# Optimization experiments

Hardware: AMD Instinct MI355X
Metric: run time of the kernel (lower is better)

## Reference

```python
import jax, jax.numpy as jnp
import numpy as np

B, C, H, W = 64, 3, 224, 224
DEPTH = 2
NUM_OPS = 14

def _lin(m, lo, hi):
    return lo + m * (hi - lo)

def _clip255(x):
    return jnp.clip(x, 0.0, 255.0)

def _affine_sample(img, a, b, c, d, e, f):
    # img: [C,H,W]; inverse map (x_out,y_out)->(a*x+b*y+c, d*x+e*y+f); bilinear, zero fill.
    ch, h, w = img.shape
    ys, xs = jnp.meshgrid(jnp.arange(h, dtype=img.dtype), jnp.arange(w, dtype=img.dtype), indexing='ij')
    sx = a * xs + b * ys + c
    sy = d * xs + e * ys + f
    x0 = jnp.floor(sx); y0 = jnp.floor(sy)
    wx = sx - x0; wy = sy - y0
    def gather(yi, xi):
        valid = (xi >= 0) & (xi <= w - 1) & (yi >= 0) & (yi <= h - 1)
        v = img[:, jnp.clip(yi, 0, h - 1).astype(jnp.int32), jnp.clip(xi, 0, w - 1).astype(jnp.int32)]
        return jnp.where(valid[None], v, 0.0)
    v00 = gather(y0, x0); v01 = gather(y0, x0 + 1)
    v10 = gather(y0 + 1, x0); v11 = gather(y0 + 1, x0 + 1)
    top = v00 * (1 - wx) + v01 * wx
    bot = v10 * (1 - wx) + v11 * wx
    return top * (1 - wy) + bot * wy

def _gray(img):
    lum = jnp.array([0.299, 0.587, 0.114], img.dtype)
    return jnp.einsum('chw,c->hw', img, lum)

def shear_x(img, m):
    v = _lin(m, -0.3, 0.3)
    return _affine_sample(img, 1.0, v, 0.0, 0.0, 1.0, 0.0)

def shear_y(img, m):
    v = _lin(m, -0.3, 0.3)
    return _affine_sample(img, 1.0, 0.0, 0.0, v, 1.0, 0.0)

def translate_x(img, m):
    v = _lin(m, -0.45, 0.45) * img.shape[2]
    return _affine_sample(img, 1.0, 0.0, v, 0.0, 1.0, 0.0)

def translate_y(img, m):
    v = _lin(m, -0.45, 0.45) * img.shape[1]
    return _affine_sample(img, 1.0, 0.0, 0.0, 0.0, 1.0, v)

def rotate(img, m):
    rad = _lin(m, -30.0, 30.0) * np.pi / 180.0
    cx = (img.shape[2] - 1) * 0.5
    cy = (img.shape[1] - 1) * 0.5
    cs, sn = jnp.cos(rad), jnp.sin(rad)
    c = cx - cs * cx - sn * cy
    f = cy + sn * cx - cs * cy
    return _affine_sample(img, cs, sn, c, -sn, cs, f)

def brightness(img, m):
    return _clip255(img * _lin(m, 0.1, 1.9))

def color(img, m):
    g = _gray(img)[None]
    return _clip255(g + _lin(m, 0.1, 1.9) * (img - g))

def sharpness(img, m):
    k = jnp.array([[1., 1., 1.], [1., 5., 1.], [1., 1., 1.]], img.dtype) / 13.0
    ch = img.shape[0]
    kern = jnp.tile(k[None, None], (ch, 1, 1, 1))  # [C,1,3,3] depthwise
    blur = jax.lax.conv_general_dilated(img[None], kern, (1, 1), 'SAME', feature_group_count=ch)[0]
    out = _clip255(blur + _lin(m, 0.1, 1.9) * (img - blur))
    # PIL keeps the 1-px border unchanged
    out = out.at[:, 0, :].set(img[:, 0, :]).at[:, -1, :].set(img[:, -1, :])
    out = out.at[:, :, 0].set(img[:, :, 0]).at[:, :, -1].set(img[:, :, -1])
    return out

def contrast(img, m):
    mu = jnp.mean(_gray(img))
    return _clip255(mu + _lin(m, 0.1, 1.9) * (img - mu))

def solarize(img, m):
    thr = _lin(m, 0.0, 256.0)
    return jnp.where(img < thr, img, 255.0 - img)

def posterize(img, m):
    nbits = jnp.round(_lin(m, 0.0, 4.0))  # bits removed -> keep 8-nbits
    q = 2.0 ** nbits
    return jnp.floor(img / q) * q

def equalize(img, m):
    def eq_ch(chan):
        v = jnp.clip(jnp.round(chan), 0, 255).astype(jnp.int32)
        hist = jnp.zeros(256, jnp.int32).at[v.ravel()].add(1)
        step = (jnp.sum(hist) - hist[255]) // 255
        cum = jnp.concatenate([jnp.zeros(1, jnp.int32), jnp.cumsum(hist)[:-1]])
        lut = jnp.where(step > 0,
                        jnp.clip((cum + step // 2) // jnp.maximum(step, 1), 0, 255),
                        jnp.arange(256))
        return lut[v].astype(chan.dtype)
    return jax.vmap(eq_ch)(img)

def autocontrast(img, m):
    lo = jnp.min(img, axis=(1, 2), keepdims=True)
    hi = jnp.max(img, axis=(1, 2), keepdims=True)
    scale = 255.0 / jnp.maximum(hi - lo, 1e-6)
    return jnp.where(hi > lo, _clip255((img - lo) * scale), img)

def identity(img, m):
    return img

BRANCHES = [shear_x, shear_y, translate_x, translate_y, rotate, brightness, color,
            sharpness, contrast, solarize, posterize, equalize, autocontrast, identity]

def setup_inputs() -> dict:
    key = jax.random.key(0)
    k1, k2, k3, k4, k5 = jax.random.split(key, 5)
    x = jax.random.uniform(k1, (B, C, H, W), jnp.float32)          # [0,1]; module scales by 255
    ra_deform = jax.random.uniform(k2, (DEPTH, B), jnp.float32)    # magnitudes in [0,1]
    op_idx = jax.random.randint(k3, (DEPTH, B), 0, NUM_OPS, jnp.int32)
    p = jax.random.uniform(k4, (DEPTH, B), jnp.float32, 0.2, 0.8)  # p_min_t..p_max_t
    apply_mask = jax.random.uniform(k5, (DEPTH, B), jnp.float32) < p
    return {"x": x, "ra_deform": ra_deform, "op_idx": op_idx, "apply_mask": apply_mask}

def reference(x, ra_deform, op_idx, apply_mask):
    x = x * jnp.where(jnp.max(x) <= 1.0, 255.0, 1.0)
    x = x.astype(jnp.float32)
    def apply_one(img, j, m, ap):
        out = jax.lax.switch(j, BRANCHES, img, m)
        return jnp.where(ap, out, img)
    for i in range(DEPTH):  # small fixed depth
        x = jax.vmap(apply_one)(x, op_idx[i], ra_deform[i], apply_mask[i])
    return jnp.clip(x / 255.0, 0.0, 1.0)
```

## Files before the change

### kernel.cpp

```cpp
#include <hip/hip_runtime.h>

#define WID 224
#define HGT 224
#define HWp (224*224)
#define CHW (3*224*224)
#define NB  64
#define ST  784
#define SPLIT 32
#define CHUNK (HWp/SPLIT)
#define BPI (CHW/1024)
#define BPC (HWp/1024)

__device__ __forceinline__ float clip255(float v){ return fminf(fmaxf(v, 0.f), 255.f); }

__device__ __forceinline__ float blk_reduce(float v, float* red, int tid, int op){
    red[tid] = v; __syncthreads();
    for (int s = 128; s > 0; s >>= 1){
        if (tid < s){
            float a = red[tid], b = red[tid+s];
            red[tid] = (op==0) ? a+b : (op==1 ? fminf(a,b) : fmaxf(a,b));
        }
        __syncthreads();
    }
    float r = red[0]; __syncthreads();
    return r;
}

__global__ void pass0_kernel(const float* __restrict__ x,
                             const int* __restrict__ op0,
                             const int* __restrict__ mask0,
                             float* __restrict__ pmaxA,
                             float* __restrict__ psum0,
                             float* __restrict__ pmin0,
                             float* __restrict__ pmax0,
                             int*   __restrict__ phist0,
                             int*   __restrict__ hist1){
    __shared__ float red[256];
    __shared__ int sh[1536];
    int blk = blockIdx.x;
    int b = blk >> 5, s = blk & 31;
    int tid = threadIdx.x;
    if (tid < 24) hist1[blk*24 + tid] = 0;

    int j = op0[b];
    int ap = mask0[b];
    bool needSum  = ap && (j == 8);
    bool needMM   = ap && (j == 12);
    bool needHist = ap && (j == 11);
    const float* img = x + (size_t)b * CHW;
    int p0 = s * CHUNK;
    const float GW[3] = {0.299f, 0.587f, 0.114f};

    float mx = 0.f, gs = 0.f;
    for (int c = 0; c < 3; c++){
        const float* pl = img + c*HWp + p0;
        float lo = 3.4e38f, hi = 0.f, csum = 0.f;
        for (int p = tid*4; p < CHUNK; p += 1024){
            float4 v = *(const float4*)(pl + p);
            float m4 = fmaxf(fmaxf(v.x, v.y), fmaxf(v.z, v.w));
            mx = fmaxf(mx, m4);
            if (needMM){ hi = fmaxf(hi, m4); lo = fminf(lo, fminf(fminf(v.x,v.y), fminf(v.z,v.w))); }
            if (needSum) csum += (v.x + v.y) + (v.z + v.w);
        }
        if (needSum) gs += GW[c] * csum;
        if (needMM){
            float l = blk_reduce(lo, red, tid, 1);
            if (tid == 0) pmin0[blk*3 + c] = l;
            float h = blk_reduce(hi, red, tid, 2);
            if (tid == 0) pmax0[blk*3 + c] = h;
        }
    }
    float bm = blk_reduce(mx, red, tid, 2);
    if (tid == 0) pmaxA[blk] = bm;
    if (needSum){
        float t = blk_reduce(gs, red, tid, 0);
        if (tid == 0) psum0[blk] = t;
    }
    if (needHist){
        for (int i = tid; i < 1536; i += 256) sh[i] = 0;
        __syncthreads();
        for (int c = 0; c < 3; c++){
            const float* pl = img + c*HWp + p0;
            for (int p = tid; p < CHUNK; p += 256){
                float v = pl[p];
                int b0 = min(max((int)rintf(v), 0), 255);
                int b1 = min(max((int)rintf(v*255.f), 0), 255);
                atomicAdd(&sh[c*256 + b0], 1);
                atomicAdd(&sh[768 + c*256 + b1], 1);
            }
        }
        __syncthreads();
        for (int i = tid; i < 1536; i += 256) phist0[blk*1536 + i] = sh[i];
    }
}

__device__ __forceinline__ void build_lut(const int* h, float* lut){
    int step = (HWp - h[255]) / 255;
    int cum = 0;
    for (int i = 0; i < 256; i++){
        int l = (step > 0) ? min(max((cum + (step >> 1)) / step, 0), 255) : i;
        lut[i] = (float)l;
        cum += h[i];
    }
}

__global__ void fin0_kernel(const int* __restrict__ op0,
                            const int* __restrict__ mask0,
                            const float* __restrict__ pmaxA,
                            const float* __restrict__ psum0,
                            const float* __restrict__ pmin0,
                            const float* __restrict__ pmax0,
                            const int*   __restrict__ phist0,
                            float* __restrict__ scalePtr,
                            float* __restrict__ stats0){
    __shared__ float red[256];
    __shared__ int h[768];
    __shared__ float sscale;
    int b = blockIdx.x, tid = threadIdx.x;
    float m = 0.f;
    for (int i = tid; i < NB*SPLIT; i += 256) m = fmaxf(m, pmaxA[i]);
    float gm = blk_reduce(m, red, tid, 2);
    if (tid == 0){
        sscale = (gm <= 1.0f) ? 255.f : 1.f;
        if (b == 0) *scalePtr = sscale;
    }
    __syncthreads();
    float scl = sscale;
    int j = op0[b];
    if (!mask0[b]) return;
    float* st = stats0 + (size_t)b * ST;
    if (j == 8){
        if (tid == 0){
            float t = 0.f;
            for (int s = 0; s < SPLIT; s++) t += psum0[b*SPLIT + s];
            st[0] = t * scl * (1.f/(float)HWp);
        }
    } else if (j == 12){
        if (tid < 3){
            float lo = 3.4e38f, hi = 0.f;
            for (int s = 0; s < SPLIT; s++){
                lo = fminf(lo, pmin0[(b*SPLIT+s)*3 + tid]);
                hi = fmaxf(hi, pmax0[(b*SPLIT+s)*3 + tid]);
            }
            st[1+tid] = lo * scl;
            st[4+tid] = hi * scl;
        }
    } else if (j == 11){
        int d = (scl == 255.f) ? 1 : 0;
        for (int i = tid; i < 768; i += 256){
            int t = 0;
            for (int s = 0; s < SPLIT; s++) t += phist0[(b*SPLIT+s)*1536 + d*768 + i];
            h[i] = t;
        }
        __syncthreads();
        if (tid < 3) build_lut(h + tid*256, st + 16 + tid*256);
    }
}

__global__ void fin1_kernel(const int* __restrict__ op1,
                            const int* __restrict__ mask1,
                            const float* __restrict__ psum1,
                            const float* __restrict__ pmin1,
                            const float* __restrict__ pmax1,
                            const int*   __restrict__ hist1,
                            float* __restrict__ stats1){
    __shared__ float red[256];
    __shared__ int h[768];
    int b = blockIdx.x, tid = threadIdx.x;
    int j = op1[b];
    if (!mask1[b]) return;
    float* st = stats1 + (size_t)b * ST;
    if (j == 8){
        float t = 0.f;
        for (int i = tid; i < BPI; i += 256) t += psum1[b*BPI + i];
        float tot = blk_reduce(t, red, tid, 0);
        if (tid == 0) st[0] = tot * (1.f/(float)HWp);
    } else if (j == 12){
        if (tid < 3){
            float lo = 3.4e38f, hi = 0.f;
            for (int k = 0; k < BPC; k++){
                lo = fminf(lo, pmin1[b*BPI + tid*BPC + k]);
                hi = fmaxf(hi, pmax1[b*BPI + tid*BPC + k]);
            }
            st[1+tid] = lo;
            st[4+tid] = hi;
        }
    } else if (j == 11){
        for (int i = tid; i < 768; i += 256) h[i] = hist1[b*768 + i];
        __syncthreads();
        if (tid < 3) build_lut(h + tid*256, st + 16 + tid*256);
    }
}

__device__ __forceinline__ float samp(const float* __restrict__ pl, float yi, float xi, float scl){
    if (xi < 0.f || xi > (float)(WID-1) || yi < 0.f || yi > (float)(HGT-1)) return 0.f;
    return pl[(int)yi * WID + (int)xi] * scl;
}

__global__ void apply_kernel(const float* __restrict__ src,
                             float* __restrict__ dst,
                             const int* __restrict__ opi,
                             const float* __restrict__ mags,
                             const int* __restrict__ mask,
                             const float* __restrict__ scalePtr,
                             const float* __restrict__ stats,
                             const int* __restrict__ opiN,
                             const int* __restrict__ maskN,
                             float* __restrict__ psumN,
                             float* __restrict__ pminN,
                             float* __restrict__ pmaxN,
                             int*   __restrict__ histN,
                             int applyScale, int finalOut, int doStats){
    __shared__ float red[256];
    __shared__ int sh[256];
    int idx = (blockIdx.x*256 + threadIdx.x) * 4;
    int tid = threadIdx.x;
    int b = idx / CHW;
    int r = idx - b*CHW;
    int c = r / HWp;
    int p = r - c*HWp;
    int y = p / WID;
    int x = p - y*WID;
    float scl = applyScale ? *scalePtr : 1.f;
    const float* img = src + (size_t)b * CHW;
    const float* pl  = img + c*HWp;
    float4 v4 = *(const float4*)(pl + p);
    float iv[4] = {v4.x*scl, v4.y*scl, v4.z*scl, v4.w*scl};
    int   j  = opi[b];
    int   ap = mask[b];
    float m  = mags[b];
    const float* st = stats + (size_t)b * ST;
    float o[4];

    if (!ap) {
        #pragma unroll
        for (int k = 0; k < 4; k++) o[k] = iv[k];
    } else {
        switch (j){
        case 0: case 1: case 2: case 3: case 4: {
            float a = 1.f, bb = 0.f, cc = 0.f, dd = 0.f, ee = 1.f, ff = 0.f;
            if (j == 0)      bb = -0.3f + 0.6f*m;
            else if (j == 1) dd = -0.3f + 0.6f*m;
            else if (j == 2) cc = (-0.45f + 0.9f*m) * (float)WID;
            else if (j == 3) ff = (-0.45f + 0.9f*m) * (float)HGT;
            else {
                float deg = -30.f + 60.f*m;
                float rad = deg * (float)(3.14159265358979323846/180.0);
                float cs = cosf(rad), sn = sinf(rad);
                float cx = (WID-1)*0.5f, cy = (HGT-1)*0.5f;
                a = cs; bb = sn; dd = -sn; ee = cs;
                cc = cx - cs*cx - sn*cy;
                ff = cy + sn*cx - cs*cy;
            }
            float yf = (float)y;
            #pragma unroll
            for (int k = 0; k < 4; k++){
                float xf = (float)(x + k);
                float sx = a*xf + bb*yf + cc;
                float sy = dd*xf + ee*yf + ff;
                float x0f = floorf(sx), y0f = floorf(sy);
                float wx = sx - x0f, wy = sy - y0f;
                float v00 = samp(pl, y0f,     x0f,     scl);
                float v01 = samp(pl, y0f,     x0f+1.f, scl);
                float v10 = samp(pl, y0f+1.f, x0f,     scl);
                float v11 = samp(pl, y0f+1.f, x0f+1.f, scl);
                float top = v00*(1.f-wx) + v01*wx;
                float bot = v10*(1.f-wx) + v11*wx;
                o[k] = top*(1.f-wy) + bot*wy;
            }
            break; }
        case 5: {
            float f = 0.1f + 1.8f*m;
            #pragma unroll
            for (int k = 0; k < 4; k++) o[k] = clip255(iv[k]*f);
            break; }
        case 6: {
            float4 r4 = *(const float4*)(img + p);
            float4 g4 = *(const float4*)(img + HWp + p);
            float4 b4 = *(const float4*)(img + 2*HWp + p);
            float rr[4] = {r4.x*scl, r4.y*scl, r4.z*scl, r4.w*scl};
            float gg[4] = {g4.x*scl, g4.y*scl, g4.z*scl, g4.w*scl};
            float bl[4] = {b4.x*scl, b4.y*scl, b4.z*scl, b4.w*scl};
            float f = 0.1f + 1.8f*m;
            #pragma unroll
            for (int k = 0; k < 4; k++){
                float g = 0.299f*rr[k] + 0.587f*gg[k] + 0.114f*bl[k];
                o[k] = clip255(g + f*(iv[k] - g));
            }
            break; }
        case 7: {
            float f = 0.1f + 1.8f*m;
            #pragma unroll
            for (int k = 0; k < 4; k++){
                int xx = x + k;
                if (y == 0 || y == HGT-1 || xx == 0 || xx == WID-1) o[k] = iv[k];
                else {
                    int q = p + k;
                    float s8 = pl[q-WID-1] + pl[q-WID] + pl[q-WID+1]
                             + pl[q-1]     + pl[q+1]
                             + pl[q+WID-1] + pl[q+WID] + pl[q+WID+1];
                    float blur = (s8*scl + 5.f*iv[k]) * (1.f/13.f);
                    o[k] = clip255(blur + f*(iv[k] - blur));
                }
            }
            break; }
        case 8: {
            float mu = st[0];
            float f = 0.1f + 1.8f*m;
            #pragma unroll
            for (int k = 0; k < 4; k++) o[k] = clip255(mu + f*(iv[k] - mu));
            break; }
        case 9: {
            float thr = 256.f*m;
            #pragma unroll
            for (int k = 0; k < 4; k++) o[k] = (iv[k] < thr) ? iv[k] : 255.f - iv[k];
            break; }
        case 10: {
            float q = exp2f(rintf(4.f*m));
            #pragma unroll
            for (int k = 0; k < 4; k++) o[k] = floorf(iv[k]/q)*q;
            break; }
        case 11: {
            #pragma unroll
            for (int k = 0; k < 4; k++){
                int ivi = min(max((int)rintf(iv[k]), 0), 255);
                o[k] = st[16 + c*256 + ivi];
            }
            break; }
        case 12: {
            float lo = st[1+c], hi = st[4+c];
            float sc = 255.f / fmaxf(hi - lo, 1e-6f);
            #pragma unroll
            for (int k = 0; k < 4; k++)
                o[k] = (hi > lo) ? clip255((iv[k] - lo) * sc) : iv[k];
            break; }
        default:
            #pragma unroll
            for (int k = 0; k < 4; k++) o[k] = iv[k];
            break;
        }
    }

    float4 w;
    if (finalOut){
        w.x = fminf(fmaxf(o[0]*(1.f/255.f), 0.f), 1.f);
        w.y = fminf(fmaxf(o[1]*(1.f/255.f), 0.f), 1.f);
        w.z = fminf(fmaxf(o[2]*(1.f/255.f), 0.f), 1.f);
        w.w = fminf(fmaxf(o[3]*(1.f/255.f), 0.f), 1.f);
    } else {
        w.x = o[0]; w.y = o[1]; w.z = o[2]; w.w = o[3];
    }
    *(float4*)(dst + idx) = w;

    if (doStats){
        int jn = opiN[b];
        if (maskN[b] && (jn == 8 || jn == 11 || jn == 12)){
            const float GW[3] = {0.299f, 0.587f, 0.114f};
            if (jn == 8){
                float s4 = (o[0] + o[1]) + (o[2] + o[3]);
                float tot = blk_reduce(s4, red, tid, 0);
                if (tid == 0) psumN[blockIdx.x] = tot * GW[c];
            } else if (jn == 12){
                float lo = fminf(fminf(o[0],o[1]), fminf(o[2],o[3]));
                float hi = fmaxf(fmaxf(o[0],o[1]), fmaxf(o[2],o[3]));
                float l = blk_reduce(lo, red, tid, 1);
                if (tid == 0) pminN[blockIdx.x] = l;
                float h = blk_reduce(hi, red, tid, 2);
                if (tid == 0) pmaxN[blockIdx.x] = h;
            } else {
                sh[tid] = 0;
                __syncthreads();
                #pragma unroll
                for (int k = 0; k < 4; k++){
                    int ivi = min(max((int)rintf(o[k]), 0), 255);
                    atomicAdd(&sh[ivi], 1);
                }
                __syncthreads();
                int v = sh[tid];
                if (v) atomicAdd(&histN[b*768 + c*256 + tid], v);
            }
        }
    }
}

extern "C" void kernel_launch(void* const* d_in, const int* in_sizes, int n_in,
                              void* d_out, int out_size, void* d_ws, size_t ws_size,
                              hipStream_t stream) {
    const float* x    = (const float*)d_in[0];
    const float* ra   = (const float*)d_in[1];
    const int*   op   = (const int*)d_in[2];
    const int*   mask = (const int*)d_in[3];
    float* out = (float*)d_out;

    float* wsf    = (float*)d_ws;
    float* scale  = wsf;
    float* pmaxA  = wsf + 64;
    float* psum0  = wsf + 2112;
    float* pmin0  = wsf + 4160;
    float* pmax0  = wsf + 10304;
    int*   phist0 = (int*)(wsf + 16448);
    int*   hist1  = (int*)(wsf + 3162176);
    float* psum1  = wsf + 3211328;
    float* pmin1  = wsf + 3220736;
    float* pmax1  = wsf + 3230144;
    float* stats0 = wsf + 3239552;
    float* stats1 = wsf + 3289728;
    float* inter  = wsf + 3342336;

    const int N = NB * CHW;

    pass0_kernel<<<NB*SPLIT, 256, 0, stream>>>(x, op, mask, pmaxA, psum0, pmin0, pmax0, phist0, hist1);
    fin0_kernel <<<NB, 256, 0, stream>>>(op, mask, pmaxA, psum0, pmin0, pmax0, phist0, scale, stats0);
    apply_kernel<<<N/1024, 256, 0, stream>>>(x, inter, op, ra, mask, scale, stats0,
                                             op + NB, mask + NB, psum1, pmin1, pmax1, hist1,
                                             1, 0, 1);
    fin1_kernel <<<NB, 256, 0, stream>>>(op + NB, mask + NB, psum1, pmin1, pmax1, hist1, stats1);
    apply_kernel<<<N/1024, 256, 0, stream>>>(inter, out, op + NB, ra + NB, mask + NB, scale, stats1,
                                             nullptr, nullptr, nullptr, nullptr, nullptr, nullptr,
                                             0, 1, 0);
}
```

Measured before the change: 163.7 us.

## Fuse all phases into one cooperative persistent kernel with grid syncs

```diff
diff --git a/kernel.cpp b/kernel.cpp
--- a/kernel.cpp
+++ b/kernel.cpp
@@ -1,4 +1,6 @@
 #include <hip/hip_runtime.h>
+#include <hip/hip_cooperative_groups.h>
+namespace cg = cooperative_groups;
 
 #define WID 224
 #define HGT 224
@@ -6,10 +8,12 @@
 #define CHW (3*224*224)
 #define NB  64
 #define ST  784
-#define SPLIT 32
-#define CHUNK (HWp/SPLIT)
-#define BPI (CHW/1024)
-#define BPC (HWp/1024)
+#define NSL 1024
+#define SL   16
+#define SCH  (HWp/SL)
+#define NT   (NB*CHW/1024)
+#define TPI  147
+#define TPC  49
 
 __device__ __forceinline__ float clip255(float v){ return fminf(fmaxf(v, 0.f), 255.f); }
 
@@ -24,74 +28,6 @@
     }
     float r = red[0]; __syncthreads();
     return r;
-}
-
-__global__ void pass0_kernel(const float* __restrict__ x,
-                             const int* __restrict__ op0,
-                             const int* __restrict__ mask0,
-                             float* __restrict__ pmaxA,
-                             float* __restrict__ psum0,
-                             float* __restrict__ pmin0,
-                             float* __restrict__ pmax0,
-                             int*   __restrict__ phist0,
-                             int*   __restrict__ hist1){
-    __shared__ float red[256];
-    __shared__ int sh[1536];
-    int blk = blockIdx.x;
-    int b = blk >> 5, s = blk & 31;
-    int tid = threadIdx.x;
-    if (tid < 24) hist1[blk*24 + tid] = 0;
-
-    int j = op0[b];
-    int ap = mask0[b];
-    bool needSum  = ap && (j == 8);
-    bool needMM   = ap && (j == 12);
-    bool needHist = ap && (j == 11);
-    const float* img = x + (size_t)b * CHW;
-    int p0 = s * CHUNK;
-    const float GW[3] = {0.299f, 0.587f, 0.114f};
-
-    float mx = 0.f, gs = 0.f;
-    for (int c = 0; c < 3; c++){
-        const float* pl = img + c*HWp + p0;
-        float lo = 3.4e38f, hi = 0.f, csum = 0.f;
-        for (int p = tid*4; p < CHUNK; p += 1024){
-            float4 v = *(const float4*)(pl + p);
-            float m4 = fmaxf(fmaxf(v.x, v.y), fmaxf(v.z, v.w));
-            mx = fmaxf(mx, m4);
-            if (needMM){ hi = fmaxf(hi, m4); lo = fminf(lo, fminf(fminf(v.x,v.y), fminf(v.z,v.w))); }
-            if (needSum) csum += (v.x + v.y) + (v.z + v.w);
-        }
-        if (needSum) gs += GW[c] * csum;
-        if (needMM){
-            float l = blk_reduce(lo, red, tid, 1);
-            if (tid == 0) pmin0[blk*3 + c] = l;
-            float h = blk_reduce(hi, red, tid, 2);
-            if (tid == 0) pmax0[blk*3 + c] = h;
-        }
-    }
-    float bm = blk_reduce(mx, red, tid, 2);
-    if (tid == 0) pmaxA[blk] = bm;
-    if (needSum){
-        float t = blk_reduce(gs, red, tid, 0);
-        if (tid == 0) psum0[blk] = t;
-    }
-    if (needHist){
-        for (int i = tid; i < 1536; i += 256) sh[i] = 0;
-        __syncthreads();
-        for (int c = 0; c < 3; c++){
-            const float* pl = img + c*HWp + p0;
-            for (int p = tid; p < CHUNK; p += 256){
-                float v = pl[p];
-                int b0 = min(max((int)rintf(v), 0), 255);
-                int b1 = min(max((int)rintf(v*255.f), 0), 255);
-                atomicAdd(&sh[c*256 + b0], 1);
-                atomicAdd(&sh[768 + c*256 + b1], 1);
-            }
-        }
-        __syncthreads();
-        for (int i = tid; i < 1536; i += 256) phist0[blk*1536 + i] = sh[i];
-    }
 }
 
 __device__ __forceinline__ void build_lut(const int* h, float* lut){
@@ -104,124 +40,28 @@
     }
 }
 
-__global__ void fin0_kernel(const int* __restrict__ op0,
-                            const int* __restrict__ mask0,
-                            const float* __restrict__ pmaxA,
-                            const float* __restrict__ psum0,
-                            const float* __restrict__ pmin0,
-                            const float* __restrict__ pmax0,
-                            const int*   __restrict__ phist0,
-                            float* __restrict__ scalePtr,
-                            float* __restrict__ stats0){
-    __shared__ float red[256];
-    __shared__ int h[768];
-    __shared__ float sscale;
-    int b = blockIdx.x, tid = threadIdx.x;
-    float m = 0.f;
-    for (int i = tid; i < NB*SPLIT; i += 256) m = fmaxf(m, pmaxA[i]);
-    float gm = blk_reduce(m, red, tid, 2);
-    if (tid == 0){
-        sscale = (gm <= 1.0f) ? 255.f : 1.f;
-        if (b == 0) *scalePtr = sscale;
-    }
-    __syncthreads();
-    float scl = sscale;
-    int j = op0[b];
-    if (!mask0[b]) return;
-    float* st = stats0 + (size_t)b * ST;
-    if (j == 8){
-        if (tid == 0){
-            float t = 0.f;
-            for (int s = 0; s < SPLIT; s++) t += psum0[b*SPLIT + s];
-            st[0] = t * scl * (1.f/(float)HWp);
-        }
-    } else if (j == 12){
-        if (tid < 3){
-            float lo = 3.4e38f, hi = 0.f;
-            for (int s = 0; s < SPLIT; s++){
-                lo = fminf(lo, pmin0[(b*SPLIT+s)*3 + tid]);
-                hi = fmaxf(hi, pmax0[(b*SPLIT+s)*3 + tid]);
-            }
-            st[1+tid] = lo * scl;
-            st[4+tid] = hi * scl;
-        }
-    } else if (j == 11){
-        int d = (scl == 255.f) ? 1 : 0;
-        for (int i = tid; i < 768; i += 256){
-            int t = 0;
-            for (int s = 0; s < SPLIT; s++) t += phist0[(b*SPLIT+s)*1536 + d*768 + i];
-            h[i] = t;
-        }
-        __syncthreads();
-        if (tid < 3) build_lut(h + tid*256, st + 16 + tid*256);
-    }
-}
-
-__global__ void fin1_kernel(const int* __restrict__ op1,
-                            const int* __restrict__ mask1,
-                            const float* __restrict__ psum1,
-                            const float* __restrict__ pmin1,
-                            const float* __restrict__ pmax1,
-                            const int*   __restrict__ hist1,
-                            float* __restrict__ stats1){
-    __shared__ float red[256];
-    __shared__ int h[768];
-    int b = blockIdx.x, tid = threadIdx.x;
-    int j = op1[b];
-    if (!mask1[b]) return;
-    float* st = stats1 + (size_t)b * ST;
-    if (j == 8){
-        float t = 0.f;
-        for (int i = tid; i < BPI; i += 256) t += psum1[b*BPI + i];
-        float tot = blk_reduce(t, red, tid, 0);
-        if (tid == 0) st[0] = tot * (1.f/(float)HWp);
-    } else if (j == 12){
-        if (tid < 3){
-            float lo = 3.4e38f, hi = 0.f;
-            for (int k = 0; k < BPC; k++){
-                lo = fminf(lo, pmin1[b*BPI + tid*BPC + k]);
-                hi = fmaxf(hi, pmax1[b*BPI + tid*BPC + k]);
-            }
-            st[1+tid] = lo;
-            st[4+tid] = hi;
-        }
-    } else if (j == 11){
-        for (int i = tid; i < 768; i += 256) h[i] = hist1[b*768 + i];
-        __syncthreads();
-        if (tid < 3) build_lut(h + tid*256, st + 16 + tid*256);
-    }
-}
-
 __device__ __forceinline__ float samp(const float* __restrict__ pl, float yi, float xi, float scl){
     if (xi < 0.f || xi > (float)(WID-1) || yi < 0.f || yi > (float)(HGT-1)) return 0.f;
     return pl[(int)yi * WID + (int)xi] * scl;
 }
 
-__global__ void apply_kernel(const float* __restrict__ src,
-                             float* __restrict__ dst,
-                             const int* __restrict__ opi,
-                             const float* __restrict__ mags,
-                             const int* __restrict__ mask,
-                             const float* __restrict__ scalePtr,
-                             const float* __restrict__ stats,
-                             const int* __restrict__ opiN,
-                             const int* __restrict__ maskN,
-                             float* __restrict__ psumN,
-                             float* __restrict__ pminN,
-                             float* __restrict__ pmaxN,
-                             int*   __restrict__ histN,
-                             int applyScale, int finalOut, int doStats){
-    __shared__ float red[256];
-    __shared__ int sh[256];
-    int idx = (blockIdx.x*256 + threadIdx.x) * 4;
-    int tid = threadIdx.x;
+__device__ __forceinline__ void apply_tile(const float* __restrict__ src,
+                                           float* __restrict__ dst,
+                                           int t, int tid,
+                                           const int* __restrict__ opi,
+                                           const float* __restrict__ mags,
+                                           const int* __restrict__ mask,
+                                           const float* __restrict__ stats,
+                                           float scl, int finalOut,
+                                           float o[4], int* ob, int* oc)
+{
+    int idx = t*1024 + tid*4;
     int b = idx / CHW;
     int r = idx - b*CHW;
     int c = r / HWp;
     int p = r - c*HWp;
     int y = p / WID;
     int x = p - y*WID;
-    float scl = applyScale ? *scalePtr : 1.f;
     const float* img = src + (size_t)b * CHW;
     const float* pl  = img + c*HWp;
     float4 v4 = *(const float4*)(pl + p);
@@ -230,7 +70,6 @@
     int   ap = mask[b];
     float m  = mags[b];
     const float* st = stats + (size_t)b * ST;
-    float o[4];
 
     if (!ap) {
         #pragma unroll
@@ -351,36 +190,265 @@
         w.x = o[0]; w.y = o[1]; w.z = o[2]; w.w = o[3];
     }
     *(float4*)(dst + idx) = w;
-
-    if (doStats){
-        int jn = opiN[b];
-        if (maskN[b] && (jn == 8 || jn == 11 || jn == 12)){
-            const float GW[3] = {0.299f, 0.587f, 0.114f};
+    *ob = b; *oc = c;
+}
+
+struct WS {
+    float* scale;
+    float* pmaxA;
+    float* psum0;
+    float* pmin0;
+    float* pmax0;
+    int*   phist0;
+    int*   hist1;
+    float* psum1;
+    float* pmin1;
+    float* pmax1;
+    float* stats0;
+    float* stats1;
+    float* inter;
+};
+__host__ __device__ __forceinline__ WS get_ws(float* wsf){
+    WS w;
+    w.scale  = wsf;
+    w.pmaxA  = wsf + 64;
+    w.psum0  = wsf + 1088;
+    w.pmin0  = wsf + 2112;
+    w.pmax0  = wsf + 5184;
+    w.phist0 = (int*)(wsf + 8256);
+    w.hist1  = (int*)(wsf + 1581120);
+    w.psum1  = wsf + 1630272;
+    w.pmin1  = wsf + 1639680;
+    w.pmax1  = wsf + 1649088;
+    w.stats0 = wsf + 1658496;
+    w.stats1 = wsf + 1708672;
+    w.inter  = wsf + 1758848;
+    return w;
+}
+
+__device__ void phase0_dev(const float* __restrict__ x, const int* __restrict__ op0,
+                           const int* __restrict__ mk0, WS w, float* red, int* sh)
+{
+    int tid = threadIdx.x;
+    for (int i = blockIdx.x*256 + tid; i < NB*768; i += gridDim.x*256) w.hist1[i] = 0;
+    const float GW[3] = {0.299f, 0.587f, 0.114f};
+    for (int wk = blockIdx.x; wk < NSL; wk += gridDim.x){
+        int b = wk >> 4, s = wk & (SL-1);
+        int j = op0[b], ap = mk0[b];
+        bool needSum  = ap && (j == 8);
+        bool needMM   = ap && (j == 12);
+        bool needHist = ap && (j == 11);
+        const float* img = x + (size_t)b * CHW;
+        int p0 = s * SCH;
+        float mx = 0.f, gs = 0.f;
+        for (int c = 0; c < 3; c++){
+            const float* pl = img + c*HWp + p0;
+            float lo = 3.4e38f, hi = 0.f, cs = 0.f;
+            for (int p = tid*4; p < SCH; p += 1024){
+                float4 v = *(const float4*)(pl + p);
+                float m4 = fmaxf(fmaxf(v.x, v.y), fmaxf(v.z, v.w));
+                mx = fmaxf(mx, m4);
+                if (needMM){ hi = fmaxf(hi, m4); lo = fminf(lo, fminf(fminf(v.x,v.y), fminf(v.z,v.w))); }
+                if (needSum) cs += (v.x + v.y) + (v.z + v.w);
+            }
+            if (needSum) gs += GW[c] * cs;
+            if (needMM){
+                float l = blk_reduce(lo, red, tid, 1);
+                if (!tid) w.pmin0[wk*3 + c] = l;
+                float h = blk_reduce(hi, red, tid, 2);
+                if (!tid) w.pmax0[wk*3 + c] = h;
+            }
+        }
+        float bm = blk_reduce(mx, red, tid, 2);
+        if (!tid) w.pmaxA[wk] = bm;
+        if (needSum){
+            float t = blk_reduce(gs, red, tid, 0);
+            if (!tid) w.psum0[wk] = t;
+        }
+        if (needHist){
+            for (int i = tid; i < 1536; i += 256) sh[i] = 0;
+            __syncthreads();
+            for (int c = 0; c < 3; c++){
+                const float* pl = img + c*HWp + p0;
+                for (int p = tid; p < SCH; p += 256){
+                    float v = pl[p];
+                    atomicAdd(&sh[c*256 + min(max((int)rintf(v), 0), 255)], 1);
+                    atomicAdd(&sh[768 + c*256 + min(max((int)rintf(v*255.f), 0), 255)], 1);
+                }
+            }
+            __syncthreads();
+            for (int i = tid; i < 1536; i += 256) w.phist0[wk*1536 + i] = sh[i];
+            __syncthreads();
+        }
+    }
+}
+
+__device__ void phase1_dev(const int* __restrict__ op0, const int* __restrict__ mk0,
+                           WS w, float* red, int* sh)
+{
+    int tid = threadIdx.x;
+    for (int b = blockIdx.x; b < NB; b += gridDim.x){
+        float m = 0.f;
+        for (int i = tid; i < NSL; i += 256) m = fmaxf(m, w.pmaxA[i]);
+        float gm = blk_reduce(m, red, tid, 2);
+        float scl = (gm <= 1.0f) ? 255.f : 1.f;
+        if (!tid && b == 0) *w.scale = scl;
+        int j = op0[b];
+        if (!mk0[b]) continue;
+        float* st = w.stats0 + (size_t)b * ST;
+        if (j == 8){
+            if (!tid){
+                float t = 0.f;
+                for (int s = 0; s < SL; s++) t += w.psum0[b*SL + s];
+                st[0] = t * scl * (1.f/(float)HWp);
+            }
+        } else if (j == 12){
+            if (tid < 3){
+                float lo = 3.4e38f, hi = 0.f;
+                for (int s = 0; s < SL; s++){
+                    lo = fminf(lo, w.pmin0[(b*SL+s)*3 + tid]);
+                    hi = fmaxf(hi, w.pmax0[(b*SL+s)*3 + tid]);
+                }
+                st[1+tid] = lo * scl;
+                st[4+tid] = hi * scl;
+            }
+        } else if (j == 11){
+            int d = (scl == 255.f) ? 1 : 0;
+            for (int i = tid; i < 768; i += 256){
+                int t = 0;
+                for (int s = 0; s < SL; s++) t += w.phist0[(b*SL+s)*1536 + d*768 + i];
+                sh[i] = t;
+            }
+            __syncthreads();
+            if (tid < 3) build_lut(sh + tid*256, st + 16 + tid*256);
+            __syncthreads();
+        }
+    }
+}
+
+__device__ void phase2_dev(const float* __restrict__ x,
+                           const float* __restrict__ ra,
+                           const int* __restrict__ op, const int* __restrict__ mask,
+                           WS w, float* red, int* sh)
+{
+    int tid = threadIdx.x;
+    const int *op0 = op, *op1 = op + NB, *mk0 = mask, *mk1 = mask + NB;
+    float scl = *w.scale;
+    const float GW[3] = {0.299f, 0.587f, 0.114f};
+    for (int t = blockIdx.x; t < NT; t += gridDim.x){
+        float o[4]; int b, c;
+        apply_tile(x, w.inter, t, tid, op0, ra, mk0, w.stats0, scl, 0, o, &b, &c);
+        int jn = op1[b];
+        if (mk1[b] && (jn == 8 || jn == 11 || jn == 12)){
             if (jn == 8){
                 float s4 = (o[0] + o[1]) + (o[2] + o[3]);
                 float tot = blk_reduce(s4, red, tid, 0);
-                if (tid == 0) psumN[blockIdx.x] = tot * GW[c];
+                if (!tid) w.psum1[t] = tot * GW[c];
             } else if (jn == 12){
                 float lo = fminf(fminf(o[0],o[1]), fminf(o[2],o[3]));
                 float hi = fmaxf(fmaxf(o[0],o[1]), fmaxf(o[2],o[3]));
                 float l = blk_reduce(lo, red, tid, 1);
-                if (tid == 0) pminN[blockIdx.x] = l;
+                if (!tid) w.pmin1[t] = l;
                 float h = blk_reduce(hi, red, tid, 2);
-                if (tid == 0) pmaxN[blockIdx.x] = h;
+                if (!tid) w.pmax1[t] = h;
             } else {
                 sh[tid] = 0;
                 __syncthreads();
                 #pragma unroll
-                for (int k = 0; k < 4; k++){
-                    int ivi = min(max((int)rintf(o[k]), 0), 255);
-                    atomicAdd(&sh[ivi], 1);
-                }
+                for (int k = 0; k < 4; k++)
+                    atomicAdd(&sh[min(max((int)rintf(o[k]), 0), 255)], 1);
                 __syncthreads();
                 int v = sh[tid];
-                if (v) atomicAdd(&histN[b*768 + c*256 + tid], v);
-            }
-        }
-    }
+                if (v) atomicAdd(&w.hist1[b*768 + c*256 + tid], v);
+                __syncthreads();
+            }
+        }
+    }
+}
+
+__device__ void phase3_dev(const int* __restrict__ op, const int* __restrict__ mask,
+                           WS w, float* red, int* sh)
+{
+    int tid = threadIdx.x;
+    const int *op1 = op + NB, *mk1 = mask + NB;
+    for (int b = blockIdx.x; b < NB; b += gridDim.x){
+        int j = op1[b];
+        if (!mk1[b]) continue;
+        float* st = w.stats1 + (size_t)b * ST;
+        if (j == 8){
+            float t = 0.f;
+            for (int i = tid; i < TPI; i += 256) t += w.psum1[b*TPI + i];
+            float tot = blk_reduce(t, red, tid, 0);
+            if (!tid) st[0] = tot * (1.f/(float)HWp);
+        } else if (j == 12){
+            if (tid < 3){
+                float lo = 3.4e38f, hi = 0.f;
+                for (int k = 0; k < TPC; k++){
+                    lo = fminf(lo, w.pmin1[b*TPI + tid*TPC + k]);
+                    hi = fmaxf(hi, w.pmax1[b*TPI + tid*TPC + k]);
+                }
+                st[1+tid] = lo;
+                st[4+tid] = hi;
+            }
+        } else if (j == 11){
+            for (int i = tid; i < 768; i += 256) sh[i] = w.hist1[b*768 + i];
+            __syncthreads();
+            if (tid < 3) build_lut(sh + tid*256, st + 16 + tid*256);
+            __syncthreads();
+        }
+    }
+}
+
+__device__ void phase4_dev(const float* __restrict__ ra,
+                           const int* __restrict__ op, const int* __restrict__ mask,
+                           float* __restrict__ out, WS w)
+{
+    int tid = threadIdx.x;
+    const int *op1 = op + NB, *mk1 = mask + NB;
+    for (int t = blockIdx.x; t < NT; t += gridDim.x){
+        float o[4]; int b, c;
+        apply_tile(w.inter, out, t, tid, op1, ra + NB, mk1, w.stats1, 1.f, 1, o, &b, &c);
+    }
+}
+
+__global__ __launch_bounds__(256, 4)
+void mega_kernel(const float* __restrict__ x, const float* __restrict__ ra,
+                 const int* __restrict__ op, const int* __restrict__ mask,
+                 float* __restrict__ out, float* __restrict__ wsf)
+{
+    __shared__ float red[256];
+    __shared__ int sh[1536];
+    WS w = get_ws(wsf);
+    cg::grid_group grid = cg::this_grid();
+    phase0_dev(x, op, mask, w, red, sh);
+    grid.sync();
+    phase1_dev(op, mask, w, red, sh);
+    grid.sync();
+    phase2_dev(x, ra, op, mask, w, red, sh);
+    grid.sync();
+    phase3_dev(op, mask, w, red, sh);
+    grid.sync();
+    phase4_dev(ra, op, mask, out, w);
+}
+
+__global__ void k_phase0(const float* x, const int* op, const int* mask, float* wsf){
+    __shared__ float red[256]; __shared__ int sh[1536];
+    phase0_dev(x, op, mask, get_ws(wsf), red, sh);
+}
+__global__ void k_phase1(const int* op, const int* mask, float* wsf){
+    __shared__ float red[256]; __shared__ int sh[1536];
+    phase1_dev(op, mask, get_ws(wsf), red, sh);
+}
+__global__ void k_phase2(const float* x, const float* ra, const int* op, const int* mask, float* wsf){
+    __shared__ float red[256]; __shared__ int sh[1536];
+    phase2_dev(x, ra, op, mask, get_ws(wsf), red, sh);
+}
+__global__ void k_phase3(const int* op, const int* mask, float* wsf){
+    __shared__ float red[256]; __shared__ int sh[1536];
+    phase3_dev(op, mask, get_ws(wsf), red, sh);
+}
+__global__ void k_phase4(const float* ra, const int* op, const int* mask, float* out, float* wsf){
+    phase4_dev(ra, op, mask, out, get_ws(wsf));
 }
 
 extern "C" void kernel_launch(void* const* d_in, const int* in_sizes, int n_in,
@@ -391,31 +459,26 @@
     const int*   op   = (const int*)d_in[2];
     const int*   mask = (const int*)d_in[3];
     float* out = (float*)d_out;
-
-    float* wsf    = (float*)d_ws;
-    float* scale  = wsf;
-    float* pmaxA  = wsf + 64;
-    float* psum0  = wsf + 2112;
-    float* pmin0  = wsf + 4160;
-    float* pmax0  = wsf + 10304;
-    int*   phist0 = (int*)(wsf + 16448);
-    int*   hist1  = (int*)(wsf + 3162176);
-    float* psum1  = wsf + 3211328;
-    float* pmin1  = wsf + 3220736;
-    float* pmax1  = wsf + 3230144;
-    float* stats0 = wsf + 3239552;
-    float* stats1 = wsf + 3289728;
-    float* inter  = wsf + 3342336;
-
-    const int N = NB * CHW;
-
-    pass0_kernel<<<NB*SPLIT, 256, 0, stream>>>(x, op, mask, pmaxA, psum0, pmin0, pmax0, phist0, hist1);
-    fin0_kernel <<<NB, 256, 0, stream>>>(op, mask, pmaxA, psum0, pmin0, pmax0, phist0, scale, stats0);
-    apply_kernel<<<N/1024, 256, 0, stream>>>(x, inter, op, ra, mask, scale, stats0,
-                                             op + NB, mask + NB, psum1, pmin1, pmax1, hist1,
-                                             1, 0, 1);
-    fin1_kernel <<<NB, 256, 0, stream>>>(op + NB, mask + NB, psum1, pmin1, pmax1, hist1, stats1);
-    apply_kernel<<<N/1024, 256, 0, stream>>>(inter, out, op + NB, ra + NB, mask + NB, scale, stats1,
-                                             nullptr, nullptr, nullptr, nullptr, nullptr, nullptr,
-                                             0, 1, 0);
-}
+    float* wsf = (float*)d_ws;
+
+    int maxPerCU = 0;
+    hipError_t qe = hipOccupancyMaxActiveBlocksPerMultiprocessor(
+        &maxPerCU, (const void*)mega_kernel, 256, 0);
+
+    hipError_t le = hipErrorUnknown;
+    if (qe == hipSuccess && maxPerCU > 0){
+        int grid = maxPerCU * 256;
+        if (grid > 1024) grid = 1024;
+        void* args[] = {(void*)&x, (void*)&ra, (void*)&op, (void*)&mask, (void*)&out, (void*)&wsf};
+        le = hipLaunchCooperativeKernel((const void*)mega_kernel,
+                                        dim3(grid), dim3(256), args, 0, stream);
+    }
+    if (le != hipSuccess){
+        (void)hipGetLastError();
+        k_phase0<<<1024, 256, 0, stream>>>(x, op, mask, wsf);
+        k_phase1<<<NB,   256, 0, stream>>>(op, mask, wsf);
+        k_phase2<<<NT,   256, 0, stream>>>(x, ra, op, mask, wsf);
+        k_phase3<<<NB,   256, 0, stream>>>(op, mask, wsf);
+        k_phase4<<<NT,   256, 0, stream>>>(ra, op, mask, out, wsf);
+    }
+}
```

Result: slower. 432.0 us (+163.9%).
